# Kernel optimization log

Hardware: AMD Instinct MI355X
Metric: run time of the kernel (lower is better)

## Reference

```python
import jax, jax.numpy as jnp
import numpy as np

B, L, D, V, T = 4, 512, 2048, 32000, 1024


def setup_inputs() -> dict:
    key = jax.random.key(0)
    k1, k2, k3 = jax.random.split(key, 3)
    encoder_outs = jax.random.normal(k1, (B, L, D), dtype=jnp.float32)
    embed_weight = jax.random.normal(k2, (V, D), dtype=jnp.float32) * 0.02
    input_ids = jax.random.randint(k3, (B, T), 0, V)
    # encoder (audio) tokens occupy the prefix of the LLM input sequence
    modality_mask = jnp.broadcast_to(jnp.arange(T) < L, (B, T))
    return {
        "encoder_outs": encoder_outs,
        "embed_weight": embed_weight,
        "input_ids": input_ids,
        "modality_mask": modality_mask,
    }


def reference(encoder_outs, embed_weight, input_ids, modality_mask):
    # chunked matmul in torch == one big contraction: (B,L,D) x (V,D) -> (B,L,V)
    sim = jnp.einsum("bld,vd->blv", encoder_outs, embed_weight)
    enc_norm = jnp.sqrt(jnp.sum(jnp.square(encoder_outs), axis=-1, keepdims=True))
    w_norm = jnp.sqrt(jnp.sum(jnp.square(embed_weight), axis=-1))  # (V,)
    cosine = sim / enc_norm / w_norm[None, None, :]
    quantize_index = jnp.argmax(cosine, axis=-1)  # (B, L)
    enc_quant = embed_weight[quantize_index]      # (B, L, D) gather lookup

    inputs_embeds = embed_weight[input_ids]       # (B, T, D)
    # pad encoder tokens to full sequence length, then blend via modality mask
    enc_pad = jnp.pad(enc_quant, ((0, 0), (0, T - L), (0, 0)))
    blended = jnp.where(modality_mask[:, :, None], enc_pad, inputs_embeds)
    return blended, quantize_index
```

## Files before the change

kernel.cpp:

```cpp
#include <hip/hip_runtime.h>
#include <math.h>

typedef __attribute__((ext_vector_type(8))) short short8v;
typedef __attribute__((ext_vector_type(4))) float f32x4;
typedef unsigned long long u64;
typedef unsigned short ushort_t;

constexpr int Bb = 4;
constexpr int Ll = 512;
constexpr int Dk = 2048;
constexpr int Vv = 32000;
constexpr int Tt = 1024;
constexpr int Mrows = Bb * Ll;

constexpr int BM = 256;
constexpr int BN = 256;
constexpr int BK = 64;
constexpr int NKT = Dk / BK;
constexpr int NBX = Mrows / BM;
constexpr int NBY = Vv / BN;
constexpr int NWG = NBX * NBY;
constexpr int CHUNK = NWG / 8;

constexpr int KCAND = 8;
constexpr int CAND_STRIDE = 500;

constexpr int FBM = 128;
constexpr int FBN = 128;
constexpr int FNVB = Vv / FBN;

constexpr size_t WS_NEEDED = 147914752ull;

__device__ __forceinline__ unsigned int fkey(float f) {
    unsigned int u = __float_as_uint(f);
    return (u & 0x80000000u) ? ~u : (u | 0x80000000u);
}
__device__ __forceinline__ void top2(u64& b1, u64& b2, u64 p) {
    if (p > b1) { b2 = b1; b1 = p; }
    else if (p > b2) { b2 = p; }
}
__device__ __forceinline__ u64 shfl64(u64 x, int m) {
    unsigned lo = __shfl_xor((unsigned)x, m, 64);
    unsigned hi = __shfl_xor((unsigned)(x >> 32), m, 64);
    return ((u64)hi << 32) | lo;
}
__device__ __forceinline__ ushort_t bftrunc(float x) {
    return (ushort_t)(__float_as_uint(x) >> 16);
}
__device__ __forceinline__ void gload_lds16(const void* g, void* l) {
    __builtin_amdgcn_global_load_lds(
        (const __attribute__((address_space(1))) unsigned int*)g,
        (__attribute__((address_space(3))) unsigned int*)l, 16, 0, 0);
}

__global__ __launch_bounds__(256) void convertA_kernel(const float* __restrict__ A,
                                                       ushort_t* __restrict__ Ab) {
    int i = blockIdx.x * blockDim.x + threadIdx.x;
    const float4* src = (const float4*)A;
    float4 x = src[i * 2], y = src[i * 2 + 1];
    ushort_t o[8] = {bftrunc(x.x), bftrunc(x.y), bftrunc(x.z), bftrunc(x.w),
                     bftrunc(y.x), bftrunc(y.y), bftrunc(y.z), bftrunc(y.w)};
    *(int4*)(Ab + (size_t)i * 8) = *(const int4*)o;
}

__global__ __launch_bounds__(256) void convertW_kernel(const float* __restrict__ W,
                                                       ushort_t* __restrict__ Wb,
                                                       float* __restrict__ winv) {
    int wave = (blockIdx.x * blockDim.x + threadIdx.x) >> 6;
    int lane = threadIdx.x & 63;
    if (wave >= Vv) return;
    const float4* row = (const float4*)(W + (size_t)wave * Dk);
    ushort4* orow = (ushort4*)(Wb + (size_t)wave * Dk);
    float s = 0.f;
#pragma unroll
    for (int i = 0; i < Dk / 4 / 64; ++i) {
        float4 v = row[lane + 64 * i];
        s = fmaf(v.x, v.x, s); s = fmaf(v.y, v.y, s);
        s = fmaf(v.z, v.z, s); s = fmaf(v.w, v.w, s);
        ushort4 o;
        o.x = bftrunc(v.x); o.y = bftrunc(v.y);
        o.z = bftrunc(v.z); o.w = bftrunc(v.w);
        orow[lane + 64 * i] = o;
    }
#pragma unroll
    for (int off = 32; off; off >>= 1) s += __shfl_down(s, off, 64);
    if (lane == 0) winv[wave] = 1.0f / sqrtf(s);
}

__global__ __launch_bounds__(256) void wnorm_kernel(const float* __restrict__ W,
                                                    float* __restrict__ winv) {
    int wave = (blockIdx.x * blockDim.x + threadIdx.x) >> 6;
    int lane = threadIdx.x & 63;
    if (wave >= Vv) return;
    const float4* row = (const float4*)(W + (size_t)wave * Dk);
    float s = 0.f;
#pragma unroll
    for (int i = 0; i < Dk / 4 / 64; ++i) {
        float4 v = row[lane + 64 * i];
        s = fmaf(v.x, v.x, s); s = fmaf(v.y, v.y, s);
        s = fmaf(v.z, v.z, s); s = fmaf(v.w, v.w, s);
    }
#pragma unroll
    for (int off = 32; off; off >>= 1) s += __shfl_down(s, off, 64);
    if (lane == 0) winv[wave] = 1.0f / sqrtf(s);
}

__global__ void init_best_kernel(u64* __restrict__ best) {
    int i = blockIdx.x * blockDim.x + threadIdx.x;
    if (i < Mrows) best[i] = 0ull;
}

__global__ __launch_bounds__(512, 2) void score_topk_kernel(
    const ushort_t* __restrict__ Ab, const ushort_t* __restrict__ Wb,
    const float* __restrict__ winv, u64* __restrict__ cand) {
    __shared__ __align__(16) ushort_t Alds[2][16384];
    __shared__ __align__(16) ushort_t Wlds[2][16384];

    const int orig = blockIdx.x;
    const int swz = (orig & 7) * CHUNK + (orig >> 3);
    const int bx = swz & (NBX - 1);
    const int by = swz >> 3;
    const int row0 = bx * BM;
    const int v0 = by * BN;

    const int tid = threadIdx.x;
    const int lane = tid & 63;
    const int w = tid >> 6;
    const int wr = w >> 2;
    const int wc = w & 3;

    const int rsub = lane & 15;
    const int ksub = (lane >> 4) * 8;

    const ushort_t* srcA[4];
    const ushort_t* srcW[4];
#pragma unroll
    for (int q = 0; q < 4; ++q) {
        const int fb = w * 4 + q, sub = fb >> 1, kk = fb & 1;
        srcA[q] = Ab + (size_t)(row0 + sub * 16 + rsub) * Dk + kk * 32 + ksub;
        srcW[q] = Wb + (size_t)(v0 + sub * 16 + rsub) * Dk + kk * 32 + ksub;
    }

    auto stage = [&](int buf, int t) {
        const int k0 = t * BK;
#pragma unroll
        for (int q = 0; q < 4; ++q) {
            const int fb = w * 4 + q;
            gload_lds16(srcA[q] + k0, &Alds[buf][fb * 512]);
            gload_lds16(srcW[q] + k0, &Wlds[buf][fb * 512]);
        }
    };

    f32x4 acc[8][4];
#pragma unroll
    for (int i = 0; i < 8; ++i)
#pragma unroll
        for (int j = 0; j < 4; ++j) acc[i][j] = (f32x4){0.f, 0.f, 0.f, 0.f};

    stage(0, 0);
    __syncthreads();
    int cur = 0;
    for (int t = 0; t < NKT; ++t) {
        if (t + 1 < NKT) stage(cur ^ 1, t + 1);
        const short8v* Ap = (const short8v*)&Alds[cur][0];
        const short8v* Wp = (const short8v*)&Wlds[cur][0];
#pragma unroll
        for (int kk = 0; kk < 2; ++kk) {
            short8v a[8], b[4];
#pragma unroll
            for (int mf = 0; mf < 8; ++mf)
                a[mf] = Ap[((wr * 8 + mf) * 2 + kk) * 64 + lane];
#pragma unroll
            for (int nf = 0; nf < 4; ++nf)
                b[nf] = Wp[((wc * 4 + nf) * 2 + kk) * 64 + lane];
            __builtin_amdgcn_s_setprio(1);
#pragma unroll
            for (int mf = 0; mf < 8; ++mf)
#pragma unroll
                for (int nf = 0; nf < 4; ++nf)
                    acc[mf][nf] = __builtin_amdgcn_mfma_f32_16x16x32_bf16(
                        a[mf], b[nf], acc[mf][nf], 0, 0, 0);
            __builtin_amdgcn_s_setprio(0);
        }
        __syncthreads();
        cur ^= 1;
    }

    const int cb = lane & 15;
    float wv[4];
#pragma unroll
    for (int nf = 0; nf < 4; ++nf) wv[nf] = winv[v0 + wc * 64 + nf * 16 + cb];

    u64(*red)[8] = (u64(*)[8]) & Alds[0][0];
#pragma unroll
    for (int mf = 0; mf < 8; ++mf) {
#pragma unroll
        for (int reg = 0; reg < 4; ++reg) {
            u64 b1 = 0, b2 = 0;
#pragma unroll
            for (int nf = 0; nf < 4; ++nf) {
                float s = acc[mf][nf][reg] * wv[nf];
                int v = v0 + wc * 64 + nf * 16 + cb;
                u64 p = ((u64)fkey(s) << 32) | (unsigned)(Vv - 1 - v);
                top2(b1, b2, p);
            }
#pragma unroll
            for (int m = 1; m < 16; m <<= 1) {
                u64 o1 = shfl64(b1, m);
                u64 o2 = shfl64(b2, m);
                top2(b1, b2, o1);
                top2(b1, b2, o2);
            }
            if (cb == 0) {
                int rl = wr * 128 + mf * 16 + ((lane >> 4) << 2) + reg;
                red[rl][wc * 2] = b1;
                red[rl][wc * 2 + 1] = b2;
            }
        }
    }
    __syncthreads();
    if (tid < BM) {
        u64 b1 = red[tid][0], b2 = red[tid][1];
#pragma unroll
        for (int j = 2; j < 8; ++j) top2(b1, b2, red[tid][j]);
        u64* c = cand + (size_t)(row0 + tid) * CAND_STRIDE + by * 2;
        c[0] = b1;
        c[1] = b2;
    }
}

template <typename LdsT>
__device__ __forceinline__ void topk_epilogue_f(f32x4 (&acc)[4][4], LdsT* ldsbase,
                                                const float* __restrict__ winv,
                                                u64* __restrict__ cand, int row0, int v0,
                                                int vby, int tid, int lane, int wr,
                                                int wc) {
    const int cbase = v0 + wc * 64 + (lane & 15);
    float wv[4];
#pragma unroll
    for (int nf = 0; nf < 4; ++nf) wv[nf] = winv[cbase + nf * 16];

    u64(*red)[4] = (u64(*)[4])ldsbase;
#pragma unroll
    for (int mf = 0; mf < 4; ++mf) {
#pragma unroll
        for (int reg = 0; reg < 4; ++reg) {
            u64 b1 = 0, b2 = 0;
#pragma unroll
            for (int nf = 0; nf < 4; ++nf) {
                float s = acc[mf][nf][reg] * wv[nf];
                int v = cbase + nf * 16;
                u64 p = ((u64)fkey(s) << 32) | (unsigned)(Vv - 1 - v);
                top2(b1, b2, p);
            }
#pragma unroll
            for (int m = 1; m < 16; m <<= 1) {
                u64 o1 = shfl64(b1, m);
                u64 o2 = shfl64(b2, m);
                top2(b1, b2, o1);
                top2(b1, b2, o2);
            }
            if ((lane & 15) == 0) {
                int rl = wr * 64 + mf * 16 + ((lane >> 4) << 2) + reg;
                red[rl][wc * 2] = b1;
                red[rl][wc * 2 + 1] = b2;
            }
        }
    }
    __syncthreads();
    if (tid < FBM) {
        u64 b1 = red[tid][0], b2 = red[tid][1];
        top2(b1, b2, red[tid][2]);
        top2(b1, b2, red[tid][3]);
        u64* c = cand + (size_t)(row0 + tid) * CAND_STRIDE + vby * 2;
        c[0] = b1;
        c[1] = b2;
    }
}

__global__ __launch_bounds__(256) void score_topk_fallback(
    const float* __restrict__ A, const float* __restrict__ W,
    const float* __restrict__ winv, u64* __restrict__ cand) {
    __shared__ __align__(16) short Albuf[4096];
    __shared__ __align__(16) short Wlbuf[4096];

    const int tid = threadIdx.x;
    const int row0 = blockIdx.x * FBM;
    const int v0 = blockIdx.y * FBN;
    const int lane = tid & 63;
    const int wid = tid >> 6;
    const int wr = wid >> 1, wc = wid & 1;

    const int rA = ((tid >> 6) << 4) + (tid & 15);
    const int kk = ((tid >> 4) & 3) * 8;

    const float* pa = A + (size_t)(row0 + rA) * Dk + kk;
    const float* pw = W + (size_t)(v0 + rA) * Dk + kk;

    float4 fa0, fa1, fa2, fa3, fw0, fw1, fw2, fw3;
    auto ld4 = [](const float* p) { return *(const float4*)p; };
    auto load_regs = [&](int k0) {
        fa0 = ld4(pa + k0); fa1 = ld4(pa + k0 + 4);
        fa2 = ld4(pa + k0 + (size_t)64 * Dk); fa3 = ld4(pa + k0 + (size_t)64 * Dk + 4);
        fw0 = ld4(pw + k0); fw1 = ld4(pw + k0 + 4);
        fw2 = ld4(pw + k0 + (size_t)64 * Dk); fw3 = ld4(pw + k0 + (size_t)64 * Dk + 4);
    };
    auto pk = [](float lo, float hi) {
        return (int)((__float_as_uint(lo) >> 16) | (__float_as_uint(hi) & 0xFFFF0000u));
    };
    auto cv = [&](float4 a, float4 b) {
        int4 r; r.x = pk(a.x, a.y); r.y = pk(a.z, a.w);
        r.z = pk(b.x, b.y); r.w = pk(b.z, b.w); return r;
    };
    auto write_lds = [&]() {
        *(int4*)(Albuf + tid * 8) = cv(fa0, fa1);
        *(int4*)(Albuf + tid * 8 + 2048) = cv(fa2, fa3);
        *(int4*)(Wlbuf + tid * 8) = cv(fw0, fw1);
        *(int4*)(Wlbuf + tid * 8 + 2048) = cv(fw2, fw3);
    };

    f32x4 acc[4][4];
#pragma unroll
    for (int i = 0; i < 4; ++i)
#pragma unroll
        for (int j = 0; j < 4; ++j) acc[i][j] = (f32x4){0.f, 0.f, 0.f, 0.f};

    load_regs(0);
    for (int kt = 0; kt < Dk / 32; ++kt) {
        write_lds();
        __syncthreads();
        if (kt + 1 < Dk / 32) load_regs((kt + 1) * 32);
        short8v af[4], bf[4];
        const short8v* Ap = (const short8v*)Albuf;
        const short8v* Wp = (const short8v*)Wlbuf;
#pragma unroll
        for (int mf = 0; mf < 4; ++mf) af[mf] = Ap[(wr * 4 + mf) * 64 + lane];
#pragma unroll
        for (int nf = 0; nf < 4; ++nf) bf[nf] = Wp[(wc * 4 + nf) * 64 + lane];
#pragma unroll
        for (int mf = 0; mf < 4; ++mf)
#pragma unroll
            for (int nf = 0; nf < 4; ++nf)
                acc[mf][nf] = __builtin_amdgcn_mfma_f32_16x16x32_bf16(
                    af[mf], bf[nf], acc[mf][nf], 0, 0, 0);
        __syncthreads();
    }

    topk_epilogue_f(acc, Albuf, winv, cand, row0, v0, blockIdx.y, tid, lane, wr, wc);
}

__global__ __launch_bounds__(256) void topk_kernel(const u64* __restrict__ cand,
                                                   int* __restrict__ sel, int nents) {
    int row = blockIdx.x * 4 + (threadIdx.x >> 6);
    int lane = threadIdx.x & 63;
    if (row >= Mrows) return;
    const u64* c = cand + (size_t)row * CAND_STRIDE;
    u64 v[8];
#pragma unroll
    for (int i = 0; i < 8; ++i) {
        int idx = lane + i * 64;
        v[i] = (idx < nents) ? c[idx] : 0ull;
    }
#pragma unroll
    for (int it = 0; it < KCAND; ++it) {
        u64 lm = 0;
#pragma unroll
        for (int i = 0; i < 8; ++i) lm = v[i] > lm ? v[i] : lm;
#pragma unroll
        for (int m = 32; m; m >>= 1) {
            u64 o = shfl64(lm, m);
            lm = o > lm ? o : lm;
        }
#pragma unroll
        for (int i = 0; i < 8; ++i)
            if (v[i] == lm) v[i] = 0;
        if (lane == 0) sel[row * KCAND + it] = Vv - 1 - (int)(unsigned)(lm & 0xFFFFFFFFu);
    }
}

__global__ __launch_bounds__(256) void rescore_kernel(
    const float* __restrict__ A, const float* __restrict__ W,
    const float* __restrict__ winv, const int* __restrict__ sel,
    u64* __restrict__ best) {
    int gw = (int)((blockIdx.x * blockDim.x + threadIdx.x) >> 6);
    int lane = threadIdx.x & 63;
    if (gw >= Mrows * KCAND) return;
    int row = gw >> 3, c = gw & 7;
    int v = sel[row * KCAND + c];
    const float4* a = (const float4*)(A + (size_t)row * Dk);
    const float4* w = (const float4*)(W + (size_t)v * Dk);
    float s = 0.f;
#pragma unroll
    for (int i = 0; i < Dk / 4 / 64; ++i) {
        float4 x = a[lane + 64 * i], y = w[lane + 64 * i];
        s = fmaf(x.x, y.x, s); s = fmaf(x.y, y.y, s);
        s = fmaf(x.z, y.z, s); s = fmaf(x.w, y.w, s);
    }
#pragma unroll
    for (int m = 32; m; m >>= 1) s += __shfl_xor(s, m, 64);
    if (lane == 0) {
        u64 p = ((u64)fkey(s * winv[v]) << 32) | (unsigned)(Vv - 1 - v);
        atomicMax(best + row, p);
    }
}

__global__ __launch_bounds__(256) void blend_kernel(
    const float* __restrict__ emb, const int* __restrict__ ids,
    const u64* __restrict__ best, float* __restrict__ out) {
    int row = blockIdx.x;
    int b = row / Tt;
    int t = row % Tt;
    int idx;
    if (t < Ll) {
        idx = Vv - 1 - (int)(best[b * Ll + t] & 0xFFFFFFFFu);
    } else {
        idx = ids[row];
    }
    const float4* src = (const float4*)(emb + (size_t)idx * Dk);
    float4* dst = (float4*)(out + (size_t)row * Dk);
    for (int i = threadIdx.x; i < Dk / 4; i += blockDim.x) dst[i] = src[i];
    if (t < Ll && threadIdx.x == 0) {
        out[(size_t)Bb * Tt * Dk + (size_t)(b * Ll + t)] = (float)idx;
    }
}

extern "C" void kernel_launch(void* const* d_in, const int* in_sizes, int n_in,
                              void* d_out, int out_size, void* d_ws, size_t ws_size,
                              hipStream_t stream) {
    const float* encoder_outs = (const float*)d_in[0];
    const float* embed_weight = (const float*)d_in[1];
    const int* input_ids = (const int*)d_in[2];

    float* out = (float*)d_out;

    float* winv = (float*)d_ws;
    u64* best = (u64*)((char*)d_ws + 131072);
    int* sel = (int*)((char*)d_ws + 147456);
    u64* cand = (u64*)((char*)d_ws + 262144);
    ushort_t* Abf = (ushort_t*)((char*)d_ws + 8454144);
    ushort_t* Wbf = (ushort_t*)((char*)d_ws + 16842752);

    init_best_kernel<<<(Mrows + 255) / 256, 256, 0, stream>>>(best);

    if (ws_size >= WS_NEEDED) {
        convertA_kernel<<<Mrows * Dk / 8 / 256, 256, 0, stream>>>(encoder_outs, Abf);
        convertW_kernel<<<Vv * 64 / 256, 256, 0, stream>>>(embed_weight, Wbf, winv);
        score_topk_kernel<<<NWG, 512, 0, stream>>>(Abf, Wbf, winv, cand);
        topk_kernel<<<Mrows / 4, 256, 0, stream>>>(cand, sel, 2 * NBY);
    } else {
        wnorm_kernel<<<Vv * 64 / 256, 256, 0, stream>>>(embed_weight, winv);
        dim3 grid(Mrows / FBM, Vv / FBN);
        score_topk_fallback<<<grid, 256, 0, stream>>>(encoder_outs, embed_weight, winv,
                                                      cand);
        topk_kernel<<<Mrows / 4, 256, 0, stream>>>(cand, sel, 2 * FNVB);
    }
    rescore_kernel<<<Mrows * KCAND / 4, 256, 0, stream>>>(encoder_outs, embed_weight,
                                                          winv, sel, best);
    blend_kernel<<<Bb * Tt, 256, 0, stream>>>(embed_weight, input_ids, best, out);
}
```

Before: 1.116 ms.

## Split GEMM K-loop into four barrier phases with interleaved partial prefetch

Restructures the bf16 MFMA main loop into four phases per K tile, each doing half the N fragments for one k-half. The global-to-LDS prefetch of the next tile is split into four pieces, one per phase. Fine-grained vmcnt waits replace the full __syncthreads, with a barrier before each phase. The aim is to spread memory issue across compute and overlap loads with MFMAs better, at the cost of more barriers and hand-placed waitcnts that must be correct for the data dependencies.

Measured after the change: 1.055 ms. -5.4%, faster.

```diff
diff --git a/kernel.cpp b/kernel.cpp
--- a/kernel.cpp
+++ b/kernel.cpp
@@ -132,23 +132,20 @@
     const int rsub = lane & 15;
     const int ksub = (lane >> 4) * 8;
 
-    const ushort_t* srcA[4];
-    const ushort_t* srcW[4];
-#pragma unroll
-    for (int q = 0; q < 4; ++q) {
-        const int fb = w * 4 + q, sub = fb >> 1, kk = fb & 1;
-        srcA[q] = Ab + (size_t)(row0 + sub * 16 + rsub) * Dk + kk * 32 + ksub;
-        srcW[q] = Wb + (size_t)(v0 + sub * 16 + rsub) * Dk + kk * 32 + ksub;
-    }
-
-    auto stage = [&](int buf, int t) {
-        const int k0 = t * BK;
-#pragma unroll
-        for (int q = 0; q < 4; ++q) {
-            const int fb = w * 4 + q;
-            gload_lds16(srcA[q] + k0, &Alds[buf][fb * 512]);
-            gload_lds16(srcW[q] + k0, &Wlds[buf][fb * 512]);
-        }
+    const ushort_t* sA0 = Ab + (size_t)(row0 + (2 * w) * 16 + rsub) * Dk + ksub;
+    const ushort_t* sA1 = Ab + (size_t)(row0 + (2 * w + 1) * 16 + rsub) * Dk + ksub;
+    const ushort_t* sW0 = Wb + (size_t)(v0 + (2 * w) * 16 + rsub) * Dk + ksub;
+    const ushort_t* sW1 = Wb + (size_t)(v0 + (2 * w + 1) * 16 + rsub) * Dk + ksub;
+
+    auto stageA = [&](int dd, int t1, int kk) {
+        const int k0 = t1 * BK + kk * 32;
+        gload_lds16(sA0 + k0, &Alds[dd][((2 * w) * 2 + kk) * 512]);
+        gload_lds16(sA1 + k0, &Alds[dd][((2 * w + 1) * 2 + kk) * 512]);
+    };
+    auto stageW = [&](int dd, int t1, int kk) {
+        const int k0 = t1 * BK + kk * 32;
+        gload_lds16(sW0 + k0, &Wlds[dd][((2 * w) * 2 + kk) * 512]);
+        gload_lds16(sW1 + k0, &Wlds[dd][((2 * w + 1) * 2 + kk) * 512]);
     };
 
     f32x4 acc[8][4];
@@ -157,34 +154,56 @@
 #pragma unroll
         for (int j = 0; j < 4; ++j) acc[i][j] = (f32x4){0.f, 0.f, 0.f, 0.f};
 
-    stage(0, 0);
+    auto phase = [&](int d, int kk, int nh, int wmode, int sop, int t1) {
+        if (wmode == 4) asm volatile("s_waitcnt vmcnt(4)" ::: "memory");
+        else if (wmode == 0) asm volatile("s_waitcnt vmcnt(0)" ::: "memory");
+        __builtin_amdgcn_s_barrier();
+        __builtin_amdgcn_sched_barrier(0);
+        asm volatile("" ::: "memory");
+
+        const short8v* Ap = (const short8v*)&Alds[d][0];
+        const short8v* Wp = (const short8v*)&Wlds[d][0];
+        short8v a[8], b[2];
+#pragma unroll
+        for (int mf = 0; mf < 8; ++mf)
+            a[mf] = Ap[((wr * 8 + mf) * 2 + kk) * 64 + lane];
+#pragma unroll
+        for (int j = 0; j < 2; ++j)
+            b[j] = Wp[((wc * 4 + nh * 2 + j) * 2 + kk) * 64 + lane];
+
+        if (sop == 0) stageA(d ^ 1, t1, 0);
+        else if (sop == 1) stageW(d ^ 1, t1, 0);
+        else if (sop == 2) stageA(d ^ 1, t1, 1);
+        else if (sop == 3) stageW(d ^ 1, t1, 1);
+
+        __builtin_amdgcn_s_setprio(1);
+#pragma unroll
+        for (int mf = 0; mf < 8; ++mf)
+#pragma unroll
+            for (int j = 0; j < 2; ++j)
+                acc[mf][nh * 2 + j] = __builtin_amdgcn_mfma_f32_16x16x32_bf16(
+                    a[mf], b[j], acc[mf][nh * 2 + j], 0, 0, 0);
+        __builtin_amdgcn_s_setprio(0);
+        __builtin_amdgcn_sched_barrier(0);
+        asm volatile("s_waitcnt lgkmcnt(0)" ::: "memory");
+    };
+
+    stageA(0, 0, 0);
+    stageW(0, 0, 0);
+    stageA(0, 0, 1);
+    stageW(0, 0, 1);
+
+    int d = 0;
+    for (int t = 0; t < NKT; ++t) {
+        const bool last = (t == NKT - 1);
+        const int t1 = t + 1;
+        phase(d, 0, 0, 4, last ? -1 : 0, t1);
+        phase(d, 0, 1, -1, last ? -1 : 1, t1);
+        phase(d, 1, 0, last ? 0 : 4, last ? -1 : 2, t1);
+        phase(d, 1, 1, -1, last ? -1 : 3, t1);
+        d ^= 1;
+    }
     __syncthreads();
-    int cur = 0;
-    for (int t = 0; t < NKT; ++t) {
-        if (t + 1 < NKT) stage(cur ^ 1, t + 1);
-        const short8v* Ap = (const short8v*)&Alds[cur][0];
-        const short8v* Wp = (const short8v*)&Wlds[cur][0];
-#pragma unroll
-        for (int kk = 0; kk < 2; ++kk) {
-            short8v a[8], b[4];
-#pragma unroll
-            for (int mf = 0; mf < 8; ++mf)
-                a[mf] = Ap[((wr * 8 + mf) * 2 + kk) * 64 + lane];
-#pragma unroll
-            for (int nf = 0; nf < 4; ++nf)
-                b[nf] = Wp[((wc * 4 + nf) * 2 + kk) * 64 + lane];
-            __builtin_amdgcn_s_setprio(1);
-#pragma unroll
-            for (int mf = 0; mf < 8; ++mf)
-#pragma unroll
-                for (int nf = 0; nf < 4; ++nf)
-                    acc[mf][nf] = __builtin_amdgcn_mfma_f32_16x16x32_bf16(
-                        a[mf], b[nf], acc[mf][nf], 0, 0, 0);
-            __builtin_amdgcn_s_setprio(0);
-        }
-        __syncthreads();
-        cur ^= 1;
-    }
 
     const int cb = lane & 15;
     float wv[4];
```

## Deepen GEMM K-loop pipeline to four LDS stages with split A/W prefetch

Applied to the files above, without the earlier changes.

Halves the K tile to 32 and uses a 4-buffer LDS ring with three tiles in flight, replacing the double-buffered loop. Each iteration splits into two half-steps that interleave the A and W global-to-LDS prefetches with MFMA blocks, using explicit vmcnt/lgkmcnt waits and raw s_barriers instead of a full __syncthreads. The aim is to hide global load latency and make better use of the matrix cores. In exchange there are more barriers per K element, and the hand-written wait counts must exactly match the number of outstanding loads to stay correct.

Result: faster. 1.034 ms (-7.3%).

```diff
diff --git a/kernel.cpp b/kernel.cpp
--- a/kernel.cpp
+++ b/kernel.cpp
@@ -15,7 +15,7 @@
 
 constexpr int BM = 256;
 constexpr int BN = 256;
-constexpr int BK = 64;
+constexpr int BK = 32;
 constexpr int NKT = Dk / BK;
 constexpr int NBX = Mrows / BM;
 constexpr int NBY = Vv / BN;
@@ -113,8 +113,8 @@
 __global__ __launch_bounds__(512, 2) void score_topk_kernel(
     const ushort_t* __restrict__ Ab, const ushort_t* __restrict__ Wb,
     const float* __restrict__ winv, u64* __restrict__ cand) {
-    __shared__ __align__(16) ushort_t Alds[2][16384];
-    __shared__ __align__(16) ushort_t Wlds[2][16384];
+    __shared__ __align__(16) ushort_t Alds[4][8192];
+    __shared__ __align__(16) ushort_t Wlds[4][8192];
 
     const int orig = blockIdx.x;
     const int swz = (orig & 7) * CHUNK + (orig >> 3);
@@ -132,23 +132,20 @@
     const int rsub = lane & 15;
     const int ksub = (lane >> 4) * 8;
 
-    const ushort_t* srcA[4];
-    const ushort_t* srcW[4];
-#pragma unroll
-    for (int q = 0; q < 4; ++q) {
-        const int fb = w * 4 + q, sub = fb >> 1, kk = fb & 1;
-        srcA[q] = Ab + (size_t)(row0 + sub * 16 + rsub) * Dk + kk * 32 + ksub;
-        srcW[q] = Wb + (size_t)(v0 + sub * 16 + rsub) * Dk + kk * 32 + ksub;
-    }
-
-    auto stage = [&](int buf, int t) {
+    const ushort_t* sA0 = Ab + (size_t)(row0 + (2 * w) * 16 + rsub) * Dk + ksub;
+    const ushort_t* sA1 = Ab + (size_t)(row0 + (2 * w + 1) * 16 + rsub) * Dk + ksub;
+    const ushort_t* sW0 = Wb + (size_t)(v0 + (2 * w) * 16 + rsub) * Dk + ksub;
+    const ushort_t* sW1 = Wb + (size_t)(v0 + (2 * w + 1) * 16 + rsub) * Dk + ksub;
+
+    auto stageA = [&](int buf, int t) {
         const int k0 = t * BK;
-#pragma unroll
-        for (int q = 0; q < 4; ++q) {
-            const int fb = w * 4 + q;
-            gload_lds16(srcA[q] + k0, &Alds[buf][fb * 512]);
-            gload_lds16(srcW[q] + k0, &Wlds[buf][fb * 512]);
-        }
+        gload_lds16(sA0 + k0, &Alds[buf][(2 * w) * 512]);
+        gload_lds16(sA1 + k0, &Alds[buf][(2 * w + 1) * 512]);
+    };
+    auto stageW = [&](int buf, int t) {
+        const int k0 = t * BK;
+        gload_lds16(sW0 + k0, &Wlds[buf][(2 * w) * 512]);
+        gload_lds16(sW1 + k0, &Wlds[buf][(2 * w + 1) * 512]);
     };
 
     f32x4 acc[8][4];
@@ -157,34 +154,59 @@
 #pragma unroll
         for (int j = 0; j < 4; ++j) acc[i][j] = (f32x4){0.f, 0.f, 0.f, 0.f};
 
-    stage(0, 0);
+    stageA(0, 0); stageW(0, 0);
+    stageA(1, 1); stageW(1, 1);
+    stageA(2, 2); stageW(2, 2);
+    asm volatile("s_waitcnt vmcnt(8)" ::: "memory");
+    __builtin_amdgcn_s_barrier();
+
+    for (int t = 0; t < NKT; ++t) {
+        const int buf = t & 3;
+        const bool st = (t + 3 < NKT);
+        const short8v* Ap = (const short8v*)&Alds[buf][0];
+        const short8v* Wp = (const short8v*)&Wlds[buf][0];
+        short8v a[4], b[4], a2[4];
+
+#pragma unroll
+        for (int i = 0; i < 4; ++i) a[i] = Ap[(wr * 8 + i) * 64 + lane];
+#pragma unroll
+        for (int j = 0; j < 4; ++j) b[j] = Wp[(wc * 4 + j) * 64 + lane];
+        if (st) stageA((t + 3) & 3, t + 3);
+        __builtin_amdgcn_s_barrier();
+        asm volatile("s_waitcnt lgkmcnt(0)" ::: "memory");
+        __builtin_amdgcn_sched_barrier(0);
+        __builtin_amdgcn_s_setprio(1);
+#pragma unroll
+        for (int i = 0; i < 4; ++i)
+#pragma unroll
+            for (int j = 0; j < 4; ++j)
+                acc[i][j] = __builtin_amdgcn_mfma_f32_16x16x32_bf16(a[i], b[j],
+                                                                    acc[i][j], 0, 0, 0);
+        __builtin_amdgcn_s_setprio(0);
+        __builtin_amdgcn_sched_barrier(0);
+        __builtin_amdgcn_s_barrier();
+
+#pragma unroll
+        for (int i = 0; i < 4; ++i) a2[i] = Ap[(wr * 8 + 4 + i) * 64 + lane];
+        if (st) stageW((t + 3) & 3, t + 3);
+        __builtin_amdgcn_s_barrier();
+        asm volatile("s_waitcnt lgkmcnt(0)" ::: "memory");
+        __builtin_amdgcn_sched_barrier(0);
+        __builtin_amdgcn_s_setprio(1);
+#pragma unroll
+        for (int i = 0; i < 4; ++i)
+#pragma unroll
+            for (int j = 0; j < 4; ++j)
+                acc[4 + i][j] = __builtin_amdgcn_mfma_f32_16x16x32_bf16(
+                    a2[i], b[j], acc[4 + i][j], 0, 0, 0);
+        __builtin_amdgcn_s_setprio(0);
+        __builtin_amdgcn_sched_barrier(0);
+        if (t <= NKT - 4) asm volatile("s_waitcnt vmcnt(8)" ::: "memory");
+        else if (t == NKT - 3) asm volatile("s_waitcnt vmcnt(4)" ::: "memory");
+        else if (t == NKT - 2) asm volatile("s_waitcnt vmcnt(0)" ::: "memory");
+        __builtin_amdgcn_s_barrier();
+    }
     __syncthreads();
-    int cur = 0;
-    for (int t = 0; t < NKT; ++t) {
-        if (t + 1 < NKT) stage(cur ^ 1, t + 1);
-        const short8v* Ap = (const short8v*)&Alds[cur][0];
-        const short8v* Wp = (const short8v*)&Wlds[cur][0];
-#pragma unroll
-        for (int kk = 0; kk < 2; ++kk) {
-            short8v a[8], b[4];
-#pragma unroll
-            for (int mf = 0; mf < 8; ++mf)
-                a[mf] = Ap[((wr * 8 + mf) * 2 + kk) * 64 + lane];
-#pragma unroll
-            for (int nf = 0; nf < 4; ++nf)
-                b[nf] = Wp[((wc * 4 + nf) * 2 + kk) * 64 + lane];
-            __builtin_amdgcn_s_setprio(1);
-#pragma unroll
-            for (int mf = 0; mf < 8; ++mf)
-#pragma unroll
-                for (int nf = 0; nf < 4; ++nf)
-                    acc[mf][nf] = __builtin_amdgcn_mfma_f32_16x16x32_bf16(
-                        a[mf], b[nf], acc[mf][nf], 0, 0, 0);
-            __builtin_amdgcn_s_setprio(0);
-        }
-        __syncthreads();
-        cur ^= 1;
-    }
 
     const int cb = lane & 15;
     float wv[4];
```

## Use 16 waves with 64x64 wave tiles and BK=32 in score GEMM

Applied to the files above, without the earlier changes.

The bf16 MFMA score kernel now launches 1024 threads per block instead of 512. Each of the 16 waves computes a 64x64 sub-tile with a 4x4 accumulator array, and the K step drops from 64 to 32. This halves both LDS usage and per-wave accumulator registers, to allow more waves in flight and better latency hiding. In exchange, each wave does fewer MFMAs per LDS fragment load, and the K loop runs twice as many iterations, each ending in a block-wide barrier.

Result: faster. 1.074 ms (-3.7%).

```diff
diff --git a/kernel.cpp b/kernel.cpp
--- a/kernel.cpp
+++ b/kernel.cpp
@@ -15,7 +15,7 @@
 
 constexpr int BM = 256;
 constexpr int BN = 256;
-constexpr int BK = 64;
+constexpr int BK = 32;
 constexpr int NKT = Dk / BK;
 constexpr int NBX = Mrows / BM;
 constexpr int NBY = Vv / BN;
@@ -110,11 +110,11 @@
     if (i < Mrows) best[i] = 0ull;
 }
 
-__global__ __launch_bounds__(512, 2) void score_topk_kernel(
+__global__ __launch_bounds__(1024, 4) void score_topk_kernel(
     const ushort_t* __restrict__ Ab, const ushort_t* __restrict__ Wb,
     const float* __restrict__ winv, u64* __restrict__ cand) {
-    __shared__ __align__(16) ushort_t Alds[2][16384];
-    __shared__ __align__(16) ushort_t Wlds[2][16384];
+    __shared__ __align__(16) ushort_t Alds[2][8192];
+    __shared__ __align__(16) ushort_t Wlds[2][8192];
 
     const int orig = blockIdx.x;
     const int swz = (orig & 7) * CHUNK + (orig >> 3);
@@ -126,62 +126,47 @@
     const int tid = threadIdx.x;
     const int lane = tid & 63;
     const int w = tid >> 6;
-    const int wr = w >> 2;
-    const int wc = w & 3;
+    const int wrr = w >> 2;
+    const int wcc = w & 3;
 
     const int rsub = lane & 15;
     const int ksub = (lane >> 4) * 8;
 
-    const ushort_t* srcA[4];
-    const ushort_t* srcW[4];
-#pragma unroll
-    for (int q = 0; q < 4; ++q) {
-        const int fb = w * 4 + q, sub = fb >> 1, kk = fb & 1;
-        srcA[q] = Ab + (size_t)(row0 + sub * 16 + rsub) * Dk + kk * 32 + ksub;
-        srcW[q] = Wb + (size_t)(v0 + sub * 16 + rsub) * Dk + kk * 32 + ksub;
-    }
-
-    auto stage = [&](int buf, int t) {
-        const int k0 = t * BK;
-#pragma unroll
-        for (int q = 0; q < 4; ++q) {
-            const int fb = w * 4 + q;
-            gload_lds16(srcA[q] + k0, &Alds[buf][fb * 512]);
-            gload_lds16(srcW[q] + k0, &Wlds[buf][fb * 512]);
-        }
-    };
-
-    f32x4 acc[8][4];
-#pragma unroll
-    for (int i = 0; i < 8; ++i)
+    const ushort_t* sA = Ab + (size_t)(row0 + w * 16 + rsub) * Dk + ksub;
+    const ushort_t* sW = Wb + (size_t)(v0 + w * 16 + rsub) * Dk + ksub;
+
+    f32x4 acc[4][4];
+#pragma unroll
+    for (int i = 0; i < 4; ++i)
 #pragma unroll
         for (int j = 0; j < 4; ++j) acc[i][j] = (f32x4){0.f, 0.f, 0.f, 0.f};
 
-    stage(0, 0);
+    gload_lds16(sA, &Alds[0][w * 512]);
+    gload_lds16(sW, &Wlds[0][w * 512]);
     __syncthreads();
+
     int cur = 0;
     for (int t = 0; t < NKT; ++t) {
-        if (t + 1 < NKT) stage(cur ^ 1, t + 1);
+        if (t + 1 < NKT) {
+            const int k0 = (t + 1) * BK;
+            gload_lds16(sA + k0, &Alds[cur ^ 1][w * 512]);
+            gload_lds16(sW + k0, &Wlds[cur ^ 1][w * 512]);
+        }
         const short8v* Ap = (const short8v*)&Alds[cur][0];
         const short8v* Wp = (const short8v*)&Wlds[cur][0];
-#pragma unroll
-        for (int kk = 0; kk < 2; ++kk) {
-            short8v a[8], b[4];
-#pragma unroll
-            for (int mf = 0; mf < 8; ++mf)
-                a[mf] = Ap[((wr * 8 + mf) * 2 + kk) * 64 + lane];
-#pragma unroll
-            for (int nf = 0; nf < 4; ++nf)
-                b[nf] = Wp[((wc * 4 + nf) * 2 + kk) * 64 + lane];
-            __builtin_amdgcn_s_setprio(1);
-#pragma unroll
-            for (int mf = 0; mf < 8; ++mf)
-#pragma unroll
-                for (int nf = 0; nf < 4; ++nf)
-                    acc[mf][nf] = __builtin_amdgcn_mfma_f32_16x16x32_bf16(
-                        a[mf], b[nf], acc[mf][nf], 0, 0, 0);
-            __builtin_amdgcn_s_setprio(0);
-        }
+        short8v a[4], b[4];
+#pragma unroll
+        for (int m = 0; m < 4; ++m) a[m] = Ap[(wrr * 4 + m) * 64 + lane];
+#pragma unroll
+        for (int n = 0; n < 4; ++n) b[n] = Wp[(wcc * 4 + n) * 64 + lane];
+        __builtin_amdgcn_s_setprio(1);
+#pragma unroll
+        for (int m = 0; m < 4; ++m)
+#pragma unroll
+            for (int n = 0; n < 4; ++n)
+                acc[m][n] = __builtin_amdgcn_mfma_f32_16x16x32_bf16(a[m], b[n],
+                                                                    acc[m][n], 0, 0, 0);
+        __builtin_amdgcn_s_setprio(0);
         __syncthreads();
         cur ^= 1;
     }
@@ -189,32 +174,32 @@
     const int cb = lane & 15;
     float wv[4];
 #pragma unroll
-    for (int nf = 0; nf < 4; ++nf) wv[nf] = winv[v0 + wc * 64 + nf * 16 + cb];
+    for (int n = 0; n < 4; ++n) wv[n] = winv[v0 + wcc * 64 + n * 16 + cb];
 
     u64(*red)[8] = (u64(*)[8]) & Alds[0][0];
 #pragma unroll
-    for (int mf = 0; mf < 8; ++mf) {
+    for (int m = 0; m < 4; ++m) {
 #pragma unroll
         for (int reg = 0; reg < 4; ++reg) {
             u64 b1 = 0, b2 = 0;
 #pragma unroll
-            for (int nf = 0; nf < 4; ++nf) {
-                float s = acc[mf][nf][reg] * wv[nf];
-                int v = v0 + wc * 64 + nf * 16 + cb;
+            for (int n = 0; n < 4; ++n) {
+                float s = acc[m][n][reg] * wv[n];
+                int v = v0 + wcc * 64 + n * 16 + cb;
                 u64 p = ((u64)fkey(s) << 32) | (unsigned)(Vv - 1 - v);
                 top2(b1, b2, p);
             }
 #pragma unroll
-            for (int m = 1; m < 16; m <<= 1) {
-                u64 o1 = shfl64(b1, m);
-                u64 o2 = shfl64(b2, m);
+            for (int msk = 1; msk < 16; msk <<= 1) {
+                u64 o1 = shfl64(b1, msk);
+                u64 o2 = shfl64(b2, msk);
                 top2(b1, b2, o1);
                 top2(b1, b2, o2);
             }
             if (cb == 0) {
-                int rl = wr * 128 + mf * 16 + ((lane >> 4) << 2) + reg;
-                red[rl][wc * 2] = b1;
-                red[rl][wc * 2 + 1] = b2;
+                int rl = wrr * 64 + m * 16 + ((lane >> 4) << 2) + reg;
+                red[rl][wcc * 2] = b1;
+                red[rl][wcc * 2 + 1] = b2;
             }
         }
     }
@@ -445,7 +430,7 @@
     if (ws_size >= WS_NEEDED) {
         convertA_kernel<<<Mrows * Dk / 8 / 256, 256, 0, stream>>>(encoder_outs, Abf);
         convertW_kernel<<<Vv * 64 / 256, 256, 0, stream>>>(embed_weight, Wbf, winv);
-        score_topk_kernel<<<NWG, 512, 0, stream>>>(Abf, Wbf, winv, cand);
+        score_topk_kernel<<<NWG, 1024, 0, stream>>>(Abf, Wbf, winv, cand);
         topk_kernel<<<Mrows / 4, 256, 0, stream>>>(cand, sel, 2 * NBY);
     } else {
         wnorm_kernel<<<Vv * 64 / 256, 256, 0, stream>>>(embed_weight, winv);
```
